# Performance work log

Hardware: AMD Instinct MI355X
Metric: run time of the kernel (lower is better)

Reference implementation:

```python
import jax, jax.numpy as jnp
import numpy as np

CHANNEL_DIM = 512
VEC_DIM = 300


def setup_inputs() -> dict:
    key = jax.random.key(0)
    k1, k2, k3 = jax.random.split(key, 3)
    h_r = jax.random.normal(k1, (256, 512, 196), dtype=jnp.float32)
    vecs = jax.random.normal(k2, (1000, VEC_DIM), dtype=jnp.float32)
    # learned parameter w_g ~ N(0,1) per nn.init.normal_
    w_g = jax.random.normal(k3, (VEC_DIM, CHANNEL_DIM), dtype=jnp.float32)
    return {"h_r": h_r, "vecs": vecs, "w_g": w_g}


def reference(h_r, vecs, w_g):
    # h_r: (b, f=512, r=196); vecs: (i, v=300); w_g: (v, f)
    h_r = h_r.reshape(-1, CHANNEL_DIM, 196)
    q = vecs @ w_g                                # (i, f)
    A = jnp.einsum('if,bfr->bir', q, h_r)         # attention logits
    A = jax.nn.softmax(A, axis=-1)
    e_g = jnp.einsum('bir,bfr->bif', A, h_r)      # (b, i, f)
    return e_g
```

## Files before the change

### kernel.cpp

```cpp
#include <hip/hip_runtime.h>

typedef _Float16 half8 __attribute__((ext_vector_type(8)));
typedef _Float16 half4 __attribute__((ext_vector_type(4)));
typedef float floatx16 __attribute__((ext_vector_type(16)));

#define MFMA(a, b, c) __builtin_amdgcn_mfma_f32_32x32x16_f16(a, b, c, 0, 0, 0)

#define NB   256
#define NF   512
#define NR   196
#define NI   1000
#define NV   300
#define IPAD 1024

#define B1S   24
#define BROWS 196
#define PS    200

__global__ __launch_bounds__(256) void qsplit_kernel(
    const float* __restrict__ vecs, const float* __restrict__ wg,
    _Float16* __restrict__ qh, _Float16* __restrict__ ql) {
    const int t = threadIdx.x;
    const int i0 = blockIdx.x * 8;
    __shared__ float vec[8][NV];
    for (int idx = t; idx < 8 * NV; idx += 256) {
        int ii = idx / NV;
        int v = idx - ii * NV;
        int i = i0 + ii;
        vec[ii][v] = (i < NI) ? vecs[(size_t)i * NV + v] : 0.0f;
    }
    __syncthreads();
    float acc[8][2];
#pragma unroll
    for (int ii = 0; ii < 8; ++ii) { acc[ii][0] = 0.f; acc[ii][1] = 0.f; }
#pragma unroll 4
    for (int v = 0; v < NV; ++v) {
        float w0 = wg[(size_t)v * NF + t];
        float w1 = wg[(size_t)v * NF + t + 256];
#pragma unroll
        for (int ii = 0; ii < 8; ++ii) {
            float x = vec[ii][v];
            acc[ii][0] += x * w0;
            acc[ii][1] += x * w1;
        }
    }
#pragma unroll
    for (int ii = 0; ii < 8; ++ii) {
        size_t i = i0 + ii;
        float q0 = acc[ii][0];
        float q1 = acc[ii][1];
        _Float16 h0 = (_Float16)q0;
        _Float16 h1 = (_Float16)q1;
        qh[i * NF + t]       = h0;
        qh[i * NF + t + 256] = h1;
        ql[i * NF + t]       = (_Float16)(q0 - (float)h0);
        ql[i * NF + t + 256] = (_Float16)(q1 - (float)h1);
    }
}

__global__ __launch_bounds__(256, 4) void attn_kernel(
    const float* __restrict__ H, const _Float16* __restrict__ qh,
    const _Float16* __restrict__ ql, float* __restrict__ out) {
    __shared__ __align__(16) char smem[37632];
    _Float16* B0h = (_Float16*)smem;
    _Float16* B0l = (_Float16*)(smem + 9408);
    _Float16* B1h = (_Float16*)(smem + 18816);
    _Float16* B1l = (_Float16*)(smem + 28224);
    _Float16* P   = (_Float16*)smem;
    float* mp = (float*)(smem + 25600);
    float* lp = (float*)(smem + 26112);

    const int tid  = threadIdx.x;
    const int lane = tid & 63;
    const int w    = tid >> 6;
    const int col  = lane & 31;
    const int hf   = lane >> 5;
    const int mt   = w >> 1;
    const int rh   = w & 1;
    const int t0   = rh * 4;
    const int ntile = rh ? 3 : 4;

    const int n      = blockIdx.x;
    const int xcd    = n & 7;
    const int slot   = n >> 3;
    const int b      = xcd + ((slot >> 4) << 3);
    const int i_base = (slot & 15) << 6;

    const float* Hb = H + (size_t)b * NF * NR;

    int goff[4], loff[4];
    bool act[4];
#pragma unroll
    for (int s = 0; s < 4; ++s) {
        int idx = s * 256 + tid;
        act[s] = idx < 4 * NR;
        int ii = act[s] ? idx : 0;
        int fg = ii / NR;
        int r  = ii - fg * NR;
        goff[s] = fg * 4 * NR + r;
        loff[s] = r * B1S + fg * 4;
    }

    float4 sx[4];

#define LOADC(c_)                                                       \
    {                                                                   \
        const float* hc = Hb + (size_t)(c_) * (16 * NR);                \
        _Pragma("unroll")                                               \
        for (int s = 0; s < 4; ++s)                                     \
            if (act[s]) {                                               \
                const float* hp = hc + goff[s];                         \
                sx[s].x = hp[0];                                        \
                sx[s].y = hp[NR];                                       \
                sx[s].z = hp[2 * NR];                                   \
                sx[s].w = hp[3 * NR];                                   \
            }                                                           \
    }

#define CONVW(bh_, bl_)                                                 \
    {                                                                   \
        _Pragma("unroll")                                               \
        for (int s = 0; s < 4; ++s)                                     \
            if (act[s]) {                                               \
                float x0 = sx[s].x, x1 = sx[s].y, x2 = sx[s].z, x3 = sx[s].w; \
                _Float16 a0 = (_Float16)x0, a1 = (_Float16)x1;          \
                _Float16 a2 = (_Float16)x2, a3 = (_Float16)x3;          \
                half4 hi = {a0, a1, a2, a3};                            \
                half4 lo = {(_Float16)(x0 - (float)a0), (_Float16)(x1 - (float)a1), \
                            (_Float16)(x2 - (float)a2), (_Float16)(x3 - (float)a3)}; \
                *(half4*)&(bh_)[loff[s]] = hi;                          \
                *(half4*)&(bl_)[loff[s]] = lo;                          \
            }                                                           \
    }

    floatx16 acc[4];
#pragma unroll
    for (int t = 0; t < 4; ++t)
#pragma unroll
        for (int k = 0; k < 16; ++k) acc[t][k] = 0.0f;

    const size_t qoff = (size_t)(i_base + 32 * mt + col) * NF;

    LOADC(0);
    CONVW(B0h, B0l);

    for (int c = 0; c < 32; ++c) {
        __syncthreads();
        if (c < 31) LOADC(c + 1);
        const _Float16* bh = (c & 1) ? B1h : B0h;
        const _Float16* bl = (c & 1) ? B1l : B0l;
        half8 a_h = *(const half8*)(qh + qoff + c * 16 + hf * 8);
        half8 a_l = *(const half8*)(ql + qoff + c * 16 + hf * 8);
#pragma unroll
        for (int t = 0; t < 4; ++t) {
            if (t < ntile) {
                int r  = (t0 + t) * 32 + col;
                int rb = r < BROWS ? r : BROWS - 1;
                half8 b_h = *(const half8*)&bh[rb * B1S + hf * 8];
                half8 b_l = *(const half8*)&bl[rb * B1S + hf * 8];
                acc[t] = MFMA(a_h, b_h, acc[t]);
                acc[t] = MFMA(a_l, b_h, acc[t]);
                acc[t] = MFMA(a_h, b_l, acc[t]);
            }
        }
        if (c < 31) {
            if (c & 1) { CONVW(B0h, B0l); } else { CONVW(B1h, B1l); }
        }
    }

    __syncthreads();

    float mx[16], sv[16];
#pragma unroll
    for (int j = 0; j < 16; ++j) {
        float m = -3.0e38f;
#pragma unroll
        for (int t = 0; t < 4; ++t) {
            if (t < ntile) {
                int r = (t0 + t) * 32 + col;
                float v = acc[t][j];
                if (r < NR) m = fmaxf(m, v);
            }
        }
#pragma unroll
        for (int s = 1; s < 32; s <<= 1) m = fmaxf(m, __shfl_xor(m, s));
        float l = 0.0f;
#pragma unroll
        for (int t = 0; t < 4; ++t) {
            if (t < ntile) {
                int r = (t0 + t) * 32 + col;
                if (r < NR) l += __expf(acc[t][j] - m);
            }
        }
#pragma unroll
        for (int s = 1; s < 32; s <<= 1) l += __shfl_xor(l, s);
        mx[j] = m;
        sv[j] = l;
    }
    if (col == 0) {
#pragma unroll
        for (int j = 0; j < 16; ++j) {
            int row = 32 * mt + (j & 3) + 8 * (j >> 2) + 4 * hf;
            mp[rh * 64 + row] = mx[j];
            lp[rh * 64 + row] = sv[j];
        }
    }
    __syncthreads();
#pragma unroll
    for (int j = 0; j < 16; ++j) {
        int row = 32 * mt + (j & 3) + 8 * (j >> 2) + 4 * hf;
        float m0 = mp[row], m1 = mp[64 + row];
        float l0 = lp[row], l1 = lp[64 + row];
        float M = fmaxf(m0, m1);
        float L = l0 * __expf(m0 - M) + l1 * __expf(m1 - M);
        float inv = 1.0f / L;
#pragma unroll
        for (int t = 0; t < 4; ++t) {
            if (t < ntile) {
                int r = (t0 + t) * 32 + col;
                if (r < PS) {
                    float p = (r < NR) ? __expf(acc[t][j] - M) * inv : 0.0f;
                    P[row * PS + r] = (_Float16)p;
                }
            }
        }
    }
    __syncthreads();

    const int myf  = rh * 32 + col;
    const int prow = (32 * mt + col) * PS;
    const size_t obase = ((size_t)b * NI + i_base) * NF;
#pragma unroll 1
    for (int fc = 0; fc < 8; ++fc) {
        const float* Hrow = Hb + (size_t)(fc * 64 + myf) * NR;
        floatx16 o0, o1;
#pragma unroll
        for (int k = 0; k < 16; ++k) { o0[k] = 0.0f; o1[k] = 0.0f; }
#pragma unroll
        for (int ks = 0; ks < 12; ++ks) {
            half8 a = *(const half8*)&P[prow + ks * 16 + hf * 8];
            const float* hp = Hrow + ks * 16 + hf * 8;
            float4 x0 = *(const float4*)hp;
            float4 x1 = *(const float4*)(hp + 4);
            half8 bb = {(_Float16)x0.x, (_Float16)x0.y, (_Float16)x0.z, (_Float16)x0.w,
                        (_Float16)x1.x, (_Float16)x1.y, (_Float16)x1.z, (_Float16)x1.w};
            if (ks & 1) o1 = MFMA(a, bb, o1);
            else        o0 = MFMA(a, bb, o0);
        }
        {
            half8 a  = {(_Float16)0.f, (_Float16)0.f, (_Float16)0.f, (_Float16)0.f,
                        (_Float16)0.f, (_Float16)0.f, (_Float16)0.f, (_Float16)0.f};
            half8 bb = a;
            if (hf == 0) {
                a = *(const half8*)&P[prow + 192];
                float4 x0 = *(const float4*)(Hrow + 192);
                bb = (half8){(_Float16)x0.x, (_Float16)x0.y, (_Float16)x0.z, (_Float16)x0.w,
                             (_Float16)0.f, (_Float16)0.f, (_Float16)0.f, (_Float16)0.f};
            }
            o0 = MFMA(a, bb, o0);
        }
        const int f = fc * 64 + myf;
#pragma unroll
        for (int j = 0; j < 16; ++j) {
            int row = 32 * mt + (j & 3) + 8 * (j >> 2) + 4 * hf;
            if (i_base + row < NI) out[obase + (size_t)row * NF + f] = o0[j] + o1[j];
        }
    }
}

extern "C" void kernel_launch(void* const* d_in, const int* in_sizes, int n_in,
                              void* d_out, int out_size, void* d_ws, size_t ws_size,
                              hipStream_t stream) {
    const float* h_r  = (const float*)d_in[0];
    const float* vecs = (const float*)d_in[1];
    const float* w_g  = (const float*)d_in[2];
    float* out = (float*)d_out;

    _Float16* qh = (_Float16*)d_ws;
    _Float16* ql = qh + (size_t)IPAD * NF;

    hipLaunchKernelGGL(qsplit_kernel, dim3(128), dim3(256), 0, stream, vecs, w_g, qh, ql);
    hipLaunchKernelGGL(attn_kernel, dim3(4096), dim3(256), 0, stream, h_r, qh, ql, out);
}
```

Before: 1.012 ms.

## Prepack h_r into MFMA-ready fp16 hi/lo tiles before the attention kernel

Adds a pre-pass kernel that converts h_r once into fp16 hi/lo split tiles laid out for the MFMA operand pattern, plus a plain fp16 copy for the second matmul. The attention kernel then loads packed half8 operands directly instead of converting fp32 h_r inside each of the 16 blocks that share a batch. Q is also stored in a matching packed layout. This trades redundant per-block conversion and strided loads for an extra pass over h_r, roughly 150MB of extra workspace traffic, and a fallback path when the workspace is too small.

Result: slower. 2.500 ms (+146.9%).

```diff
diff --git a/kernel.cpp b/kernel.cpp
--- a/kernel.cpp
+++ b/kernel.cpp
@@ -13,9 +13,236 @@
 #define NV   300
 #define IPAD 1024
 
+#define PKC  3584
+#define PS    200
 #define B1S   24
 #define BROWS 196
-#define PS    200
+
+
+__global__ __launch_bounds__(256) void packh_kernel(
+    const float* __restrict__ H, _Float16* __restrict__ Bh2,
+    _Float16* __restrict__ Bl2, _Float16* __restrict__ Hf) {
+    const int n = blockIdx.x;
+    const int b = n >> 5;
+    const int c = n & 31;
+    const int tid = threadIdx.x;
+    __shared__ float tile[16][200];
+    const float* src = H + ((size_t)b * NF + c * 16) * NR;
+    _Float16* hfdst = Hf + ((size_t)b * NF + c * 16) * NR;
+    for (int idx = tid; idx < 16 * NR; idx += 256) {
+        int fl = idx / NR;
+        int r  = idx - fl * NR;
+        float x = src[(size_t)fl * NR + r];
+        tile[fl][r] = x;
+        hfdst[(size_t)fl * NR + r] = (_Float16)x;
+    }
+    __syncthreads();
+    if (tid < 224) {
+        const int r = tid;
+        __align__(16) _Float16 hi[16];
+        __align__(16) _Float16 lo[16];
+#pragma unroll
+        for (int k = 0; k < 16; ++k) {
+            float x = (r < NR) ? tile[k][r] : 0.0f;
+            _Float16 h = (_Float16)x;
+            hi[k] = h;
+            lo[k] = (_Float16)(x - (float)h);
+        }
+        size_t base = (size_t)n * PKC + (size_t)tid * 16;
+        *(half8*)&Bh2[base]     = *(half8*)&hi[0];
+        *(half8*)&Bh2[base + 8] = *(half8*)&hi[8];
+        *(half8*)&Bl2[base]     = *(half8*)&lo[0];
+        *(half8*)&Bl2[base + 8] = *(half8*)&lo[8];
+    }
+}
+
+__global__ __launch_bounds__(256) void qsplit_pk_kernel(
+    const float* __restrict__ vecs, const float* __restrict__ wg,
+    _Float16* __restrict__ qh, _Float16* __restrict__ ql) {
+    const int t = threadIdx.x;
+    const int i0 = blockIdx.x * 8;
+    __shared__ float vec[8][NV];
+    for (int idx = t; idx < 8 * NV; idx += 256) {
+        int ii = idx / NV;
+        int v = idx - ii * NV;
+        int i = i0 + ii;
+        vec[ii][v] = (i < NI) ? vecs[(size_t)i * NV + v] : 0.0f;
+    }
+    __syncthreads();
+    float acc[8][2];
+#pragma unroll
+    for (int ii = 0; ii < 8; ++ii) { acc[ii][0] = 0.f; acc[ii][1] = 0.f; }
+#pragma unroll 4
+    for (int v = 0; v < NV; ++v) {
+        float w0 = wg[(size_t)v * NF + t];
+        float w1 = wg[(size_t)v * NF + t + 256];
+#pragma unroll
+        for (int ii = 0; ii < 8; ++ii) {
+            float x = vec[ii][v];
+            acc[ii][0] += x * w0;
+            acc[ii][1] += x * w1;
+        }
+    }
+#pragma unroll
+    for (int ii = 0; ii < 8; ++ii) {
+        int i = i0 + ii;
+#pragma unroll
+        for (int half = 0; half < 2; ++half) {
+            int f = t + half * 256;
+            float q = acc[ii][half];
+            _Float16 h = (_Float16)q;
+            size_t off = ((size_t)(i >> 5) * 32 + (f >> 4)) * 512 + (size_t)(i & 31) * 16 + (f & 15);
+            qh[off] = h;
+            ql[off] = (_Float16)(q - (float)h);
+        }
+    }
+}
+
+__global__ __launch_bounds__(256, 6) void attn_pk_kernel(
+    const _Float16* __restrict__ Bh2, const _Float16* __restrict__ Bl2,
+    const _Float16* __restrict__ Hf, const _Float16* __restrict__ qh,
+    const _Float16* __restrict__ ql, float* __restrict__ out) {
+    __shared__ __align__(16) char smem[26624];
+    _Float16* P = (_Float16*)smem;
+    float* mp = (float*)(smem + 25600);
+    float* lp = (float*)(smem + 26112);
+
+    const int tid  = threadIdx.x;
+    const int lane = tid & 63;
+    const int w    = tid >> 6;
+    const int col  = lane & 31;
+    const int hf   = lane >> 5;
+    const int mt   = w >> 1;
+    const int rh   = w & 1;
+    const int t0   = rh * 4;
+    const int ntile = rh ? 3 : 4;
+
+    const int n      = blockIdx.x;
+    const int xcd    = n & 7;
+    const int slot   = n >> 3;
+    const int b      = xcd + ((slot >> 4) << 3);
+    const int i_base = (slot & 15) << 6;
+
+    const int lo16 = col * 16 + hf * 8;
+    const size_t hb2  = (size_t)b * 32 * PKC;
+    const size_t qoff = ((size_t)((i_base >> 5) + mt) * 32) * 512 + lo16;
+
+    floatx16 acc[4];
+#pragma unroll
+    for (int t = 0; t < 4; ++t)
+#pragma unroll
+        for (int k = 0; k < 16; ++k) acc[t][k] = 0.0f;
+
+    for (int c = 0; c < 32; ++c) {
+        const _Float16* bh = Bh2 + hb2 + (size_t)c * PKC;
+        const _Float16* bl = Bl2 + hb2 + (size_t)c * PKC;
+        half8 a_h = *(const half8*)(qh + qoff + (size_t)c * 512);
+        half8 a_l = *(const half8*)(ql + qoff + (size_t)c * 512);
+#pragma unroll
+        for (int t = 0; t < 4; ++t) {
+            if (t < ntile) {
+                half8 b_h = *(const half8*)(bh + (t0 + t) * 512 + lo16);
+                half8 b_l = *(const half8*)(bl + (t0 + t) * 512 + lo16);
+                acc[t] = MFMA(a_h, b_h, acc[t]);
+                acc[t] = MFMA(a_l, b_h, acc[t]);
+                acc[t] = MFMA(a_h, b_l, acc[t]);
+            }
+        }
+    }
+
+    float mx[16], sv[16];
+#pragma unroll
+    for (int j = 0; j < 16; ++j) {
+        float m = -3.0e38f;
+#pragma unroll
+        for (int t = 0; t < 4; ++t) {
+            if (t < ntile) {
+                int r = (t0 + t) * 32 + col;
+                float v = acc[t][j];
+                if (r < NR) m = fmaxf(m, v);
+            }
+        }
+#pragma unroll
+        for (int s = 1; s < 32; s <<= 1) m = fmaxf(m, __shfl_xor(m, s));
+        float l = 0.0f;
+#pragma unroll
+        for (int t = 0; t < 4; ++t) {
+            if (t < ntile) {
+                int r = (t0 + t) * 32 + col;
+                if (r < NR) l += __expf(acc[t][j] - m);
+            }
+        }
+#pragma unroll
+        for (int s = 1; s < 32; s <<= 1) l += __shfl_xor(l, s);
+        mx[j] = m;
+        sv[j] = l;
+    }
+    if (col == 0) {
+#pragma unroll
+        for (int j = 0; j < 16; ++j) {
+            int row = 32 * mt + (j & 3) + 8 * (j >> 2) + 4 * hf;
+            mp[rh * 64 + row] = mx[j];
+            lp[rh * 64 + row] = sv[j];
+        }
+    }
+    __syncthreads();
+#pragma unroll
+    for (int j = 0; j < 16; ++j) {
+        int row = 32 * mt + (j & 3) + 8 * (j >> 2) + 4 * hf;
+        float m0 = mp[row], m1 = mp[64 + row];
+        float l0 = lp[row], l1 = lp[64 + row];
+        float M = fmaxf(m0, m1);
+        float L = l0 * __expf(m0 - M) + l1 * __expf(m1 - M);
+        float inv = 1.0f / L;
+#pragma unroll
+        for (int t = 0; t < 4; ++t) {
+            if (t < ntile) {
+                int r = (t0 + t) * 32 + col;
+                if (r < PS) {
+                    float p = (r < NR) ? __expf(acc[t][j] - M) * inv : 0.0f;
+                    P[row * PS + r] = (_Float16)p;
+                }
+            }
+        }
+    }
+    __syncthreads();
+
+    const int myf  = rh * 32 + col;
+    const int prow = (32 * mt + col) * PS;
+    const size_t obase = ((size_t)b * NI + i_base) * NF;
+    const _Float16* Hb16 = Hf + (size_t)b * NF * NR;
+#pragma unroll 1
+    for (int fc = 0; fc < 8; ++fc) {
+        const _Float16* Hrow = Hb16 + (size_t)(fc * 64 + myf) * NR;
+        floatx16 o0, o1;
+#pragma unroll
+        for (int k = 0; k < 16; ++k) { o0[k] = 0.0f; o1[k] = 0.0f; }
+#pragma unroll
+        for (int ks = 0; ks < 12; ++ks) {
+            half8 a  = *(const half8*)&P[prow + ks * 16 + hf * 8];
+            half8 bb = *(const half8*)(Hrow + ks * 16 + hf * 8);
+            if (ks & 1) o1 = MFMA(a, bb, o1);
+            else        o0 = MFMA(a, bb, o0);
+        }
+        {
+            half8 a  = {(_Float16)0.f, (_Float16)0.f, (_Float16)0.f, (_Float16)0.f,
+                        (_Float16)0.f, (_Float16)0.f, (_Float16)0.f, (_Float16)0.f};
+            half8 bb = a;
+            if (hf == 0) {
+                a  = *(const half8*)&P[prow + 192];
+                bb = *(const half8*)(Hrow + 192);
+            }
+            o0 = MFMA(a, bb, o0);
+        }
+        const int f = fc * 64 + myf;
+#pragma unroll
+        for (int j = 0; j < 16; ++j) {
+            int row = 32 * mt + (j & 3) + 8 * (j >> 2) + 4 * hf;
+            if (i_base + row < NI) out[obase + (size_t)row * NF + f] = o0[j] + o1[j];
+        }
+    }
+}
+
 
 __global__ __launch_bounds__(256) void qsplit_kernel(
     const float* __restrict__ vecs, const float* __restrict__ wg,
@@ -276,9 +503,25 @@
     const float* w_g  = (const float*)d_in[2];
     float* out = (float*)d_out;
 
+    const size_t HQ   = (size_t)IPAD * NF;
+    const size_t HB2  = (size_t)NB * 32 * PKC;
+    const size_t HFSZ = (size_t)NB * NF * NR + 8;
+    const size_t need_bytes = (2 * HQ + 2 * HB2 + HFSZ) * sizeof(_Float16);
+
     _Float16* qh = (_Float16*)d_ws;
-    _Float16* ql = qh + (size_t)IPAD * NF;
-
-    hipLaunchKernelGGL(qsplit_kernel, dim3(128), dim3(256), 0, stream, vecs, w_g, qh, ql);
-    hipLaunchKernelGGL(attn_kernel, dim3(4096), dim3(256), 0, stream, h_r, qh, ql, out);
+
+    if (ws_size >= need_bytes) {
+        _Float16* ql  = qh + HQ;
+        _Float16* Bh2 = ql + HQ;
+        _Float16* Bl2 = Bh2 + HB2;
+        _Float16* Hf  = Bl2 + HB2;
+        hipLaunchKernelGGL(packh_kernel, dim3(NB * 32), dim3(256), 0, stream, h_r, Bh2, Bl2, Hf);
+        hipLaunchKernelGGL(qsplit_pk_kernel, dim3(128), dim3(256), 0, stream, vecs, w_g, qh, ql);
+        hipLaunchKernelGGL(attn_pk_kernel, dim3(4096), dim3(256), 0, stream,
+                           Bh2, Bl2, Hf, qh, ql, out);
+    } else {
+        _Float16* ql = qh + HQ;
+        hipLaunchKernelGGL(qsplit_kernel, dim3(128), dim3(256), 0, stream, vecs, w_g, qh, ql);
+        hipLaunchKernelGGL(attn_kernel, dim3(4096), dim3(256), 0, stream, h_r, qh, ql, out);
+    }
 }
```
